# Kernel optimization log

Hardware: AMD Instinct MI355X
Metric: run time of the kernel (lower is better)

Reference implementation:

```python
import jax, jax.numpy as jnp
import numpy as np

K = 2
LAMBDA_ALPHA = 1.0
LAMBDA_BETA = 0.5


def setup_inputs() -> dict:
    key = jax.random.key(0)
    k1, k2, k3, k4, k5 = jax.random.split(key, 5)
    bs, C, H, W = 32, 256, 64, 64
    R = 8
    hid = C // R  # 32
    x = jax.random.normal(k1, (bs, C, H, W), dtype=jnp.float32)
    # fc1: Linear(C -> C/R)
    w1 = jax.random.normal(k2, (hid, C), dtype=jnp.float32) * 0.05
    b1 = jnp.zeros((hid,), dtype=jnp.float32)
    # fc2: k Linears(hid -> 2C), stacked on leading k axis
    w2 = jax.random.normal(k3, (K, 2 * C, hid), dtype=jnp.float32) * 0.05
    b2 = jax.random.normal(k4, (K, 2 * C), dtype=jnp.float32) * 0.05
    return {"x": x, "w1": w1, "b1": b1, "w2": w2, "b2": b2}


def reference(x, w1, b1, w2, b2):
    # Residual branch: global avg pool -> fc1 -> relu -> k fc2 heads -> 2*sigmoid-1
    pooled = x.mean(axis=(2, 3))                       # [bs, C]
    h = jax.nn.relu(pooled @ w1.T + b1)                # [bs, hid]
    delta = 2.0 * jax.nn.sigmoid(
        jnp.einsum('koh,bh->bko', w2, h) + b2[None]) - 1.0  # [bs, k, 2C]
    alpha = delta[..., 0::2]                           # [bs, k, C] (even cols)
    beta = delta[..., 1::2]                            # [bs, k, C] (odd cols)
    init_alpha = jnp.array([1.0, 0.0], dtype=x.dtype)  # init_alpha[0]=1
    init_beta = jnp.array([1.0, 0.0], dtype=x.dtype)   # init_beta[0]=1 (as in source)
    a = init_alpha[None, :, None] + LAMBDA_ALPHA * alpha  # [bs, k, C]
    b = init_beta[None, :, None] + LAMBDA_BETA * beta     # [bs, k, C]
    # broadcasted per-(b,c) affine, max over k branches
    y = x[:, None] * a[..., None, None] + b[..., None, None]  # [bs, k, C, H, W]
    return jnp.max(y, axis=1)                                  # [bs, C, H, W]
```

## Files before the change

### kernel.cpp

```cpp
#include <hip/hip_runtime.h>


#define BS   32
#define CCH  256
#define HW   4096
#define HID  32
#define KK   2

__global__ __launch_bounds__(256) void pool_kernel(const float* __restrict__ x,
                                                   float* __restrict__ pooled) {
    const int bc = blockIdx.x;
    const float4* xp = (const float4*)(x + (size_t)bc * HW);
    const int t = threadIdx.x;
    float s = 0.f;
#pragma unroll
    for (int i = 0; i < 4; ++i) {
        float4 v = xp[t + i * 256];
        s += (v.x + v.y) + (v.z + v.w);
    }
#pragma unroll
    for (int off = 32; off > 0; off >>= 1)
        s += __shfl_down(s, off, 64);
    __shared__ float ws[4];
    if ((t & 63) == 0) ws[t >> 6] = s;
    __syncthreads();
    if (t == 0) {
        float tot = (ws[0] + ws[1]) + (ws[2] + ws[3]);
        pooled[bc] = tot * (1.0f / HW);
    }
}

__global__ __launch_bounds__(256) void coef_kernel(const float* __restrict__ pooled,
                                                   const float* __restrict__ w1,
                                                   const float* __restrict__ b1,
                                                   const float* __restrict__ w2,
                                                   const float* __restrict__ b2,
                                                   float* __restrict__ A,
                                                   float* __restrict__ Bc) {
    const int b = blockIdx.x;
    const int t = threadIdx.x;
    __shared__ float pl[CCH];
    __shared__ float h[HID];
    if (t < CCH) pl[t] = pooled[b * CCH + t];
    __syncthreads();
    if (t < HID) {
        float s = b1[t];
        const float* w1r = w1 + t * CCH;
        for (int c = 0; c < CCH; ++c) s += pl[c] * w1r[c];
        h[t] = s > 0.f ? s : 0.f;
    }
    __syncthreads();
    for (int idx = t; idx < KK * 2 * CCH; idx += 256) {
        const int k = idx >> 9;
        const int o = idx & 511;
        float s = b2[k * 2 * CCH + o];
        const float* w2p = w2 + (size_t)(k * 2 * CCH + o) * HID;
#pragma unroll
        for (int j = 0; j < HID; ++j) s += w2p[j] * h[j];
        const float d = 2.f / (1.f + expf(-s)) - 1.f;
        const int c = o >> 1;
        const float initv = (k == 0) ? 1.f : 0.f;
        if ((o & 1) == 0)
            A[(b * KK + k) * CCH + c] = initv + 1.0f * d;
        else
            Bc[(b * KK + k) * CCH + c] = initv + 0.5f * d;
    }
}

__global__ __launch_bounds__(256) void apply_kernel(const float* __restrict__ x,
                                                    const float* __restrict__ A,
                                                    const float* __restrict__ Bc,
                                                    float* __restrict__ out) {
    const size_t i4 = (size_t)blockIdx.x * 256 + threadIdx.x;
    const int bc = (int)(i4 >> 10);
    const int b = bc >> 8;
    const int c = bc & 255;
    const float a0 = A[(b * 2 + 0) * CCH + c];
    const float a1 = A[(b * 2 + 1) * CCH + c];
    const float b0 = Bc[(b * 2 + 0) * CCH + c];
    const float b1 = Bc[(b * 2 + 1) * CCH + c];
    const float4 v = ((const float4*)x)[i4];
    float4 r;
    r.x = fmaxf(v.x * a0 + b0, v.x * a1 + b1);
    r.y = fmaxf(v.y * a0 + b0, v.y * a1 + b1);
    r.z = fmaxf(v.z * a0 + b0, v.z * a1 + b1);
    r.w = fmaxf(v.w * a0 + b0, v.w * a1 + b1);
    ((float4*)out)[i4] = r;
}

extern "C" void kernel_launch(void* const* d_in, const int* in_sizes, int n_in,
                              void* d_out, int out_size, void* d_ws, size_t ws_size,
                              hipStream_t stream) {
    const float* x  = (const float*)d_in[0];
    const float* w1 = (const float*)d_in[1];
    const float* b1 = (const float*)d_in[2];
    const float* w2 = (const float*)d_in[3];
    const float* b2 = (const float*)d_in[4];
    float* out = (float*)d_out;

    float* pooled = (float*)d_ws;
    float* A      = pooled + BS * CCH;
    float* Bc     = A + BS * KK * CCH;

    pool_kernel<<<BS * CCH, 256, 0, stream>>>(x, pooled);
    coef_kernel<<<BS, 256, 0, stream>>>(pooled, w1, b1, w2, b2, A, Bc);
    const int n4 = (BS * CCH * HW) / 4;
    apply_kernel<<<n4 / 256, 256, 0, stream>>>(x, A, Bc, out);
}
```

Measured before the change: 260.4 us.

## Use per-channel apply blocks with nontemporal IO and parallelize fc1 reduction

The apply kernel now launches one block per (batch, channel) plane. Each thread handles four float4 elements, so the coefficients are loaded once per block. Loads and stores use nontemporal builtins to avoid cache pollution on a streaming pass. The fc1 matvec in coef_kernel is split across 8 lanes per hidden unit with a shuffle reduction, where only 32 threads did the work before. The nontemporal load of x may lose L2/MALL reuse from the pool pass, which read x just before.

```diff
diff --git a/kernel.cpp b/kernel.cpp
--- a/kernel.cpp
+++ b/kernel.cpp
@@ -6,6 +6,8 @@
 #define HW   4096
 #define HID  32
 #define KK   2
+
+typedef float f4 __attribute__((ext_vector_type(4)));
 
 __global__ __launch_bounds__(256) void pool_kernel(const float* __restrict__ x,
                                                    float* __restrict__ pooled) {
@@ -41,13 +43,20 @@
     const int t = threadIdx.x;
     __shared__ float pl[CCH];
     __shared__ float h[HID];
-    if (t < CCH) pl[t] = pooled[b * CCH + t];
+    pl[t] = pooled[b * CCH + t];
     __syncthreads();
-    if (t < HID) {
-        float s = b1[t];
-        const float* w1r = w1 + t * CCH;
-        for (int c = 0; c < CCH; ++c) s += pl[c] * w1r[c];
-        h[t] = s > 0.f ? s : 0.f;
+    {
+        const int j = t >> 3;
+        const int l8 = t & 7;
+        const float* w1r = w1 + j * CCH + l8 * 32;
+        const float* plr = pl + l8 * 32;
+        float s = 0.f;
+#pragma unroll
+        for (int cdx = 0; cdx < 32; ++cdx) s += plr[cdx] * w1r[cdx];
+#pragma unroll
+        for (int off = 4; off > 0; off >>= 1)
+            s += __shfl_down(s, off, 8);
+        if (l8 == 0) h[j] = fmaxf(s + b1[j], 0.f);
     }
     __syncthreads();
     for (int idx = t; idx < KK * 2 * CCH; idx += 256) {
@@ -71,21 +80,26 @@
                                                     const float* __restrict__ A,
                                                     const float* __restrict__ Bc,
                                                     float* __restrict__ out) {
-    const size_t i4 = (size_t)blockIdx.x * 256 + threadIdx.x;
-    const int bc = (int)(i4 >> 10);
+    const int bc = blockIdx.x;
     const int b = bc >> 8;
     const int c = bc & 255;
     const float a0 = A[(b * 2 + 0) * CCH + c];
     const float a1 = A[(b * 2 + 1) * CCH + c];
     const float b0 = Bc[(b * 2 + 0) * CCH + c];
     const float b1 = Bc[(b * 2 + 1) * CCH + c];
-    const float4 v = ((const float4*)x)[i4];
-    float4 r;
-    r.x = fmaxf(v.x * a0 + b0, v.x * a1 + b1);
-    r.y = fmaxf(v.y * a0 + b0, v.y * a1 + b1);
-    r.z = fmaxf(v.z * a0 + b0, v.z * a1 + b1);
-    r.w = fmaxf(v.w * a0 + b0, v.w * a1 + b1);
-    ((float4*)out)[i4] = r;
+    const f4* __restrict__ xp = (const f4*)(x + (size_t)bc * HW);
+    f4* __restrict__ op = (f4*)(out + (size_t)bc * HW);
+    const int t = threadIdx.x;
+#pragma unroll
+    for (int i = 0; i < 4; ++i) {
+        const f4 v = __builtin_nontemporal_load(&xp[t + i * 256]);
+        f4 r;
+        r.x = fmaxf(v.x * a0 + b0, v.x * a1 + b1);
+        r.y = fmaxf(v.y * a0 + b0, v.y * a1 + b1);
+        r.z = fmaxf(v.z * a0 + b0, v.z * a1 + b1);
+        r.w = fmaxf(v.w * a0 + b0, v.w * a1 + b1);
+        __builtin_nontemporal_store(r, &op[t + i * 256]);
+    }
 }
 
 extern "C" void kernel_launch(void* const* d_in, const int* in_sizes, int n_in,
@@ -104,6 +118,5 @@
 
     pool_kernel<<<BS * CCH, 256, 0, stream>>>(x, pooled);
     coef_kernel<<<BS, 256, 0, stream>>>(pooled, w1, b1, w2, b2, A, Bc);
-    const int n4 = (BS * CCH * HW) / 4;
-    apply_kernel<<<n4 / 256, 256, 0, stream>>>(x, A, Bc, out);
+    apply_kernel<<<BS * CCH, 256, 0, stream>>>(x, A, Bc, out);
 }
```

Result: no change. 258.2 us (-0.8%).
